# Optimization experiments

Measured on AMD Instinct MI355X. Metric: run time of the kernel, lower is better.

Reference implementation:

```python
import jax, jax.numpy as jnp
import numpy as np

N_NODES = 100000


def _gcn_layer(h_in, W, b, src, dst, norm, num_nodes):
    # PyG GCNConv: linear transform first, then normalized scatter-add aggregation
    h = h_in @ W                                   # [N, out_dim]
    msg = h[src] * norm[:, None]                   # gather + scale over edges
    out = jax.ops.segment_sum(msg, dst, num_segments=num_nodes)
    return out + b


def setup_inputs() -> dict:
    key = jax.random.key(0)
    k1, k2, k3, k4, k5 = jax.random.split(key, 5)
    d_in, d_hid, d_out = 128, 128, 128
    x = jax.random.normal(k1, (N_NODES, d_in), dtype=jnp.float32)
    edge_index = jax.random.randint(k2, (2, 1600000), 0, N_NODES, dtype=jnp.int64)
    # Glorot-ish init for weights, zeros for bias (as in GCNConv defaults)
    W1 = jax.random.normal(k3, (d_in, d_hid), dtype=jnp.float32) / np.sqrt(d_in)
    b1 = jnp.zeros((d_hid,), dtype=jnp.float32)
    W2 = jax.random.normal(k4, (d_hid, d_out), dtype=jnp.float32) / np.sqrt(d_hid)
    b2 = jnp.zeros((d_out,), dtype=jnp.float32)
    return {"x": x, "edge_index": edge_index, "W1": W1, "b1": b1, "W2": W2, "b2": b2}


def reference(x, edge_index, W1, b1, W2, b2):
    num_nodes = x.shape[0]
    # Add self-loops (GCNConv default add_self_loops=True)
    loop = jnp.arange(num_nodes, dtype=edge_index.dtype)
    src = jnp.concatenate([edge_index[0], loop])
    dst = jnp.concatenate([edge_index[1], loop])
    # Symmetric normalization: deg^{-1/2}[src] * deg^{-1/2}[dst]
    deg = jax.ops.segment_sum(jnp.ones_like(dst, dtype=x.dtype), dst, num_segments=num_nodes)
    dinv = jnp.where(deg > 0, jax.lax.rsqrt(deg), 0.0)
    norm = dinv[src] * dinv[dst]                   # [E + N]

    h = _gcn_layer(x, W1, b1, src, dst, norm, num_nodes)
    h = jax.nn.relu(h)                             # dropout is identity in eval mode
    out = _gcn_layer(h, W2, b2, src, dst, norm, num_nodes)
    return out
```

## Files before the change

### kernel.cpp

```cpp
#include <hip/hip_runtime.h>


#define DIM 128
#define CAP 192
typedef unsigned short ushort_t;
typedef unsigned int uint_t;
typedef __attribute__((ext_vector_type(8))) short bf16x8;
typedef __attribute__((ext_vector_type(4))) float f32x4;
typedef __attribute__((ext_vector_type(2))) float f32x2;

static __device__ __forceinline__ uint_t f2bf(float f) {
    union { float f; uint_t u; } c; c.f = f;
    uint_t u = c.u;
    return (u + 0x7FFFu + ((u >> 16) & 1u)) >> 16;
}
static __device__ __forceinline__ float bf2f(uint_t h) {
    union { uint_t u; float f; } c; c.u = h << 16;
    return c.f;
}
static __device__ __forceinline__ float as_f(uint_t u) {
    union { uint_t u; float f; } c; c.u = u;
    return c.f;
}
static __device__ __forceinline__ void gld16(const void* g, void* l) {
    __builtin_amdgcn_global_load_lds(
        (const __attribute__((address_space(1))) uint_t*)g,
        (__attribute__((address_space(3))) uint_t*)l, 16, 0, 0);
}

__global__ __launch_bounds__(256) void k_bin(const int* __restrict__ src,
                                             const int* __restrict__ dst,
                                             int* __restrict__ bcur,
                                             uint_t* __restrict__ stage,
                                             int E, int RB) {
    int e = blockIdx.x * 256 + threadIdx.x;
    if (e >= E) return;
    int slice = blockIdx.x & 31;
    int s = src[e], d = dst[e];
    int idx = slice * RB + (d >> 7);
    int c = atomicAdd(&bcur[idx], 1);
    if (c < CAP)
        stage[(size_t)idx * CAP + c] = (uint_t)((s << 7) | (d & 127));
}

__global__ __launch_bounds__(1024) void k_bscan(const int* __restrict__ bcur,
                                                int* __restrict__ bbase, int RB) {
    __shared__ int sdat[1024];
    int t = threadIdx.x;
    int v = 0;
    if (t < RB)
        #pragma unroll
        for (int s = 0; s < 32; ++s) v += min(bcur[s * RB + t], CAP);
    sdat[t] = v;
    __syncthreads();
    #pragma unroll
    for (int o = 1; o < 1024; o <<= 1) {
        int x = (t >= o) ? sdat[t - o] : 0;
        __syncthreads();
        sdat[t] += x;
        __syncthreads();
    }
    if (t < RB) bbase[t] = sdat[t] - v;
}

__global__ __launch_bounds__(256) void k_build(const uint_t* __restrict__ stage,
                                               const int* __restrict__ bcur,
                                               const int* __restrict__ bbase,
                                               int* __restrict__ off,
                                               float* __restrict__ dinv,
                                               int* __restrict__ csr_src,
                                               int RB, int N, int E) {
    __shared__ int scnt[33];
    __shared__ int cnt[128], excl[128], lcur[128];
    __shared__ uint_t ent[32 * CAP];
    int b = blockIdx.x, t = threadIdx.x;
    if (t < 32) scnt[t + 1] = min(bcur[t * RB + b], CAP);
    if (t == 0) scnt[0] = 0;
    if (t < 128) { cnt[t] = 0; lcur[t] = 0; }
    __syncthreads();
    if (t == 0)
        for (int s = 1; s <= 32; ++s) scnt[s] += scnt[s - 1];
    __syncthreads();
    int total = scnt[32];
    for (int s = 0; s < 32; ++s) {
        int c0 = scnt[s], c1 = scnt[s + 1];
        const uint_t* sp = stage + (size_t)(s * RB + b) * CAP - c0;
        for (int i = c0 + t; i < c1; i += 256) ent[i] = sp[i];
    }
    __syncthreads();
    for (int i = t; i < total; i += 256) atomicAdd(&cnt[ent[i] & 127], 1);
    __syncthreads();
    if (t < 128) excl[t] = cnt[t];
    __syncthreads();
    #pragma unroll
    for (int o = 1; o < 128; o <<= 1) {
        int x = 0;
        if (t < 128 && t >= o) x = excl[t - o];
        __syncthreads();
        if (t < 128) excl[t] += x;
        __syncthreads();
    }
    int base = bbase[b];
    if (t < 128) {
        excl[t] -= cnt[t];
        int node = (b << 7) + t;
        if (node < N) {
            off[node] = base + excl[t];
            dinv[node] = rsqrtf((float)cnt[t] + 1.0f);
        }
    }
    if (b == RB - 1 && t == 0) off[N] = E;
    __syncthreads();
    for (int i = t; i < total; i += 256) {
        uint_t v = ent[i];
        int dl = v & 127;
        int pos = base + excl[dl] + atomicAdd(&lcur[dl], 1);
        csr_src[pos] = (int)(v >> 7);
    }
}

__global__ __launch_bounds__(256) void k_prep(const float* __restrict__ W1,
                                              const float* __restrict__ W2,
                                              const float* __restrict__ x,
                                              short* __restrict__ whi,
                                              short* __restrict__ wlo,
                                              short* __restrict__ xhi,
                                              short* __restrict__ xlo,
                                              int N, int nxc) {
    int t = threadIdx.x;
    if (blockIdx.x < 16) {
        int g = blockIdx.x * 256 + t;
        int layer = g >> 11, c = g & 2047;
        const float* W = layer ? W2 : W1;
        int ks = c >> 9, nt = (c >> 6) & 7, l = c & 63;
        int q = l >> 4, m = l & 15;
        int n = nt * 16 + m;
        bf16x8 h8, l8;
        #pragma unroll
        for (int j = 0; j < 8; ++j) {
            int k = ks * 32 + q * 8 + j;
            float f = W[k * 128 + n];
            uint_t hb = f2bf(f);
            h8[j] = (short)hb;
            l8[j] = (short)f2bf(f - bf2f(hb));
        }
        ((bf16x8*)whi)[g] = h8;
        ((bf16x8*)wlo)[g] = l8;
    } else {
        int c = (blockIdx.x - 16) * 256 + t;
        if (c >= nxc) return;
        int rb = c >> 11, row = (c >> 4) & 127, cc = c & 15;
        int node = rb * 128 + row;
        bf16x8 h8 = {}, l8 = {};
        if (node < N) {
            f32x4 fa = __builtin_nontemporal_load((const f32x4*)x + node * 32 + cc * 2);
            f32x4 fb = __builtin_nontemporal_load((const f32x4*)x + node * 32 + cc * 2 + 1);
            float f[8] = {fa[0], fa[1], fa[2], fa[3], fb[0], fb[1], fb[2], fb[3]};
            #pragma unroll
            for (int j = 0; j < 8; ++j) {
                uint_t hb = f2bf(f[j]);
                h8[j] = (short)hb;
                l8[j] = (short)f2bf(f[j] - bf2f(hb));
            }
        }
        int pos = (cc & 8) | ((cc & 7) ^ (row & 7));
        int slot = rb * 2048 + row * 16 + pos;
        __builtin_nontemporal_store(h8, (bf16x8*)xhi + slot);
        __builtin_nontemporal_store(l8, (bf16x8*)xlo + slot);
    }
}

__global__ __launch_bounds__(256) void k_gemm(const short* __restrict__ afhi,
                                              const short* __restrict__ aflo,
                                              const short* __restrict__ wfhi,
                                              const short* __restrict__ wflo,
                                              const float* __restrict__ dinv,
                                              ushort_t* __restrict__ hout, int M) {
    __shared__ short AH[8192], AL[8192], WH[8192], WL[8192];
    const int t = threadIdx.x;
    const int rb = blockIdx.x;
    const int wv = t >> 6, l = t & 63;
    const int mb = (wv & 1) * 4;
    const int nbc = (wv >> 1) * 4;

    f32x4 acc[4][4];
    #pragma unroll
    for (int i = 0; i < 4; ++i)
        #pragma unroll
        for (int j = 0; j < 4; ++j)
            acc[i][j] = (f32x4){0.f, 0.f, 0.f, 0.f};

    #pragma unroll
    for (int kc = 0; kc < 2; ++kc) {
        if (kc) __syncthreads();
        {
            const short* ga = afhi + (size_t)rb * 16384;
            const short* gb = aflo + (size_t)rb * 16384;
            const short* gh = wfhi + 2 * kc * 4096;
            const short* gl = wflo + 2 * kc * 4096;
            #pragma unroll
            for (int i = 0; i < 4; ++i) {
                int idx = i * 256 + t;
                int goff = ((idx >> 3) * 16 + kc * 8 + (idx & 7)) * 8;
                gld16(ga + goff, AH + idx * 8);
                gld16(gb + goff, AL + idx * 8);
                gld16(gh + idx * 8, WH + idx * 8);
                gld16(gl + idx * 8, WL + idx * 8);
            }
        }
        __syncthreads();
        #pragma unroll
        for (int ksl = 0; ksl < 2; ++ksl) {
            bf16x8 ah[4], al[4];
            #pragma unroll
            for (int i = 0; i < 4; ++i) {
                int rowl = (mb + i) * 16 + (l & 15);
                int cA = ksl * 4 + (l >> 4);
                int sa = rowl * 64 + ((cA ^ (rowl & 7)) << 3);
                ah[i] = *(const bf16x8*)&AH[sa];
                al[i] = *(const bf16x8*)&AL[sa];
            }
            #pragma unroll
            for (int j = 0; j < 4; ++j) {
                bf16x8 bh = *(const bf16x8*)&WH[((ksl * 8 + nbc + j) * 64 + l) * 8];
                bf16x8 bl = *(const bf16x8*)&WL[((ksl * 8 + nbc + j) * 64 + l) * 8];
                #pragma unroll
                for (int i = 0; i < 4; ++i) {
                    acc[i][j] = __builtin_amdgcn_mfma_f32_16x16x32_bf16(ah[i], bh, acc[i][j], 0, 0, 0);
                    acc[i][j] = __builtin_amdgcn_mfma_f32_16x16x32_bf16(al[i], bh, acc[i][j], 0, 0, 0);
                    acc[i][j] = __builtin_amdgcn_mfma_f32_16x16x32_bf16(ah[i], bl, acc[i][j], 0, 0, 0);
                }
            }
        }
    }

    const int q = l >> 4, mm = l & 15;
    #pragma unroll
    for (int i = 0; i < 4; ++i)
        #pragma unroll
        for (int r = 0; r < 4; ++r) {
            int gr = rb * 128 + (wv & 1) * 64 + i * 16 + q * 4 + r;
            if (gr < M) {
                float di = dinv[gr];
                #pragma unroll
                for (int j = 0; j < 4; ++j)
                    hout[gr * 128 + nbc * 16 + j * 16 + mm] =
                        (ushort_t)f2bf(di * acc[i][j][r]);
            }
        }
}

template <int FRAG>
__global__ __launch_bounds__(256) void k_agg(const uint_t* __restrict__ h32,
                                             const int* __restrict__ off,
                                             const int* __restrict__ csr_src,
                                             const float* __restrict__ dinv,
                                             const float* __restrict__ bias,
                                             float* __restrict__ out,
                                             uint_t* __restrict__ fhi,
                                             uint_t* __restrict__ flo, int N) {
    int n = (blockIdx.x * 256 + threadIdx.x) >> 6;
    if (n >= N) return;
    int l = threadIdx.x & 63;
    const uint_t* hl = h32 + l;

    float di = dinv[n];
    f32x2 bv = *((const f32x2*)bias + l);
    uint_t sv = hl[(size_t)n << 6];
    float accx = as_f(sv << 16);
    float accy = as_f(sv & 0xffff0000u);

    int e = off[n], end = off[n + 1];
    for (; e + 16 <= end; e += 16) {
        int s[16]; uint_t v[16];
        #pragma unroll
        for (int u = 0; u < 16; ++u) s[u] = __builtin_nontemporal_load(&csr_src[e + u]);
        #pragma unroll
        for (int u = 0; u < 16; ++u) v[u] = hl[(size_t)s[u] << 6];
        #pragma unroll
        for (int u = 0; u < 16; ++u) {
            accx += as_f(v[u] << 16);
            accy += as_f(v[u] & 0xffff0000u);
        }
    }
    if (e + 8 <= end) {
        int s[8]; uint_t v[8];
        #pragma unroll
        for (int u = 0; u < 8; ++u) s[u] = __builtin_nontemporal_load(&csr_src[e + u]);
        #pragma unroll
        for (int u = 0; u < 8; ++u) v[u] = hl[(size_t)s[u] << 6];
        #pragma unroll
        for (int u = 0; u < 8; ++u) {
            accx += as_f(v[u] << 16);
            accy += as_f(v[u] & 0xffff0000u);
        }
        e += 8;
    }
    for (; e < end; ++e) {
        uint_t v = hl[(size_t)csr_src[e] << 6];
        accx += as_f(v << 16);
        accy += as_f(v & 0xffff0000u);
    }

    accx = di * accx + bv.x;
    accy = di * accy + bv.y;

    if (FRAG) {
        accx = fmaxf(accx, 0.f);
        accy = fmaxf(accy, 0.f);
        uint_t hx = f2bf(accx), hy = f2bf(accy);
        uint_t lx = f2bf(accx - bf2f(hx)), ly = f2bf(accy - bf2f(hy));
        int rb = n >> 7, row = n & 127, cc = l >> 2;
        int pos = (cc & 8) | ((cc & 7) ^ (row & 7));
        size_t iu = ((size_t)rb << 13) + row * 64 + pos * 4 + (l & 3);
        __builtin_nontemporal_store((hy << 16) | hx, &fhi[iu]);
        __builtin_nontemporal_store((ly << 16) | lx, &flo[iu]);
    } else {
        f32x2 o; o.x = accx; o.y = accy;
        __builtin_nontemporal_store(o, (f32x2*)out + ((size_t)n << 6) + l);
    }
}

extern "C" void kernel_launch(void* const* d_in, const int* in_sizes, int n_in,
                              void* d_out, int out_size, void* d_ws, size_t ws_size,
                              hipStream_t stream) {
    const float* x  = (const float*)d_in[0];
    const int*   ei = (const int*)d_in[1];
    const float* W1 = (const float*)d_in[2];
    const float* b1 = (const float*)d_in[3];
    const float* W2 = (const float*)d_in[4];
    const float* b2 = (const float*)d_in[5];
    float* out = (float*)d_out;

    const int N = in_sizes[0] / DIM;
    const int E = in_sizes[1] / 2;
    const int* src = ei;
    const int* dst = ei + E;
    const int RB = (N + 127) / 128;
    const int nxc = RB * 2048;

    char* w = (char*)d_ws;
    float* dinv    = (float*)(w);
    int*   bcur    = (int*)  (w + (1 << 19));
    int*   bbase   = (int*)  (w + (1 << 19) + (1 << 17));
    int*   off     = (int*)  (w + (3 << 19));
    short* whi     = (short*)(w + (1 << 21) + (1 << 13));
    short* wlo     = whi + 2 * 16384;
    int*   csr_src = (int*)  (w + ((size_t)5 << 19));
    short* fhi     = (short*)(w + ((size_t)17 << 20));
    short* flo     = (short*)(w + ((size_t)43 << 20));
    ushort_t* hbuf = (ushort_t*)(w + ((size_t)69 << 20));
    uint_t* stage  = (uint_t*)hbuf;

    const int B = 256;
    const int agg_grid = (N * 64 + B - 1) / B;

    hipMemsetAsync(bcur, 0, (size_t)32 * RB * 4, stream);
    k_prep<<<16 + (nxc + B - 1) / B, B, 0, stream>>>(W1, W2, x, whi, wlo,
                                                     fhi, flo, N, nxc);
    k_bin<<<(E + B - 1) / B, B, 0, stream>>>(src, dst, bcur, stage, E, RB);
    k_bscan<<<1, 1024, 0, stream>>>(bcur, bbase, RB);
    k_build<<<RB, B, 0, stream>>>(stage, bcur, bbase, off, dinv, csr_src,
                                  RB, N, E);
    k_gemm<<<RB, B, 0, stream>>>(fhi, flo, whi, wlo, dinv, hbuf, N);
    k_agg<1><<<agg_grid, B, 0, stream>>>((const uint_t*)hbuf, off, csr_src,
                                         dinv, b1, nullptr,
                                         (uint_t*)fhi, (uint_t*)flo, N);
    k_gemm<<<RB, B, 0, stream>>>(fhi, flo, whi + 16384, wlo + 16384, dinv, hbuf, N);
    k_agg<0><<<agg_grid, B, 0, stream>>>((const uint_t*)hbuf, off, csr_src,
                                         dinv, b2, out,
                                         nullptr, nullptr, N);
}
```

Baseline: 408.4 us.

## Split aggregation wave into two edge halves with 8-byte gathers; reorder A tiles by k-chunk

The aggregation kernel now has each 64-lane wave handle two edges per step. Each half-wave gathers a full 256-byte bf16 row using 8-byte loads per lane, and the two halves are combined with a cross-half shuffle at the end. The goal is fewer load instructions and more independent gathers in flight per wave. The fragment layout written by the conversion and aggregation kernels is also reorganised so each GEMM k-chunk is contiguous, letting the GEMM tile loads use plain linear offsets. In exchange, half the lanes sit idle in the epilogue and the shuffle reduction adds some work.

```diff
diff --git a/kernel.cpp b/kernel.cpp
--- a/kernel.cpp
+++ b/kernel.cpp
@@ -8,6 +8,7 @@
 typedef __attribute__((ext_vector_type(8))) short bf16x8;
 typedef __attribute__((ext_vector_type(4))) float f32x4;
 typedef __attribute__((ext_vector_type(2))) float f32x2;
+typedef __attribute__((ext_vector_type(2))) unsigned int u32x2;
 
 static __device__ __forceinline__ uint_t f2bf(float f) {
     union { float f; uint_t u; } c; c.f = f;
@@ -163,8 +164,7 @@
                 l8[j] = (short)f2bf(f[j] - bf2f(hb));
             }
         }
-        int pos = (cc & 8) | ((cc & 7) ^ (row & 7));
-        int slot = rb * 2048 + row * 16 + pos;
+        int slot = rb * 2048 + (cc >> 3) * 1024 + row * 8 + ((cc & 7) ^ (row & 7));
         __builtin_nontemporal_store(h8, (bf16x8*)xhi + slot);
         __builtin_nontemporal_store(l8, (bf16x8*)xlo + slot);
     }
@@ -194,18 +194,17 @@
     for (int kc = 0; kc < 2; ++kc) {
         if (kc) __syncthreads();
         {
-            const short* ga = afhi + (size_t)rb * 16384;
-            const short* gb = aflo + (size_t)rb * 16384;
-            const short* gh = wfhi + 2 * kc * 4096;
-            const short* gl = wflo + 2 * kc * 4096;
+            const short* ga = afhi + (size_t)rb * 16384 + kc * 8192;
+            const short* gb = aflo + (size_t)rb * 16384 + kc * 8192;
+            const short* gh = wfhi + kc * 8192;
+            const short* gl = wflo + kc * 8192;
             #pragma unroll
             for (int i = 0; i < 4; ++i) {
-                int idx = i * 256 + t;
-                int goff = ((idx >> 3) * 16 + kc * 8 + (idx & 7)) * 8;
-                gld16(ga + goff, AH + idx * 8);
-                gld16(gb + goff, AL + idx * 8);
-                gld16(gh + idx * 8, WH + idx * 8);
-                gld16(gl + idx * 8, WL + idx * 8);
+                int idx = (i * 256 + t) * 8;
+                gld16(ga + idx, AH + idx);
+                gld16(gb + idx, AL + idx);
+                gld16(gh + idx, WH + idx);
+                gld16(gl + idx, WL + idx);
             }
         }
         __syncthreads();
@@ -262,62 +261,73 @@
     int n = (blockIdx.x * 256 + threadIdx.x) >> 6;
     if (n >= N) return;
     int l = threadIdx.x & 63;
-    const uint_t* hl = h32 + l;
+    int half = l >> 5, c = l & 31;
+    const u32x2* hrow = (const u32x2*)h32 + c;
+
+    float ax = 0.f, ay = 0.f, az = 0.f, aw = 0.f;
+    if (!half) {
+        u32x2 sv = hrow[(size_t)n * 32];
+        ax = as_f(sv.x << 16); ay = as_f(sv.x & 0xffff0000u);
+        az = as_f(sv.y << 16); aw = as_f(sv.y & 0xffff0000u);
+    }
+
+    int e = off[n], end = off[n + 1];
+    for (; e + 32 <= end; e += 32) {
+        int s[16]; u32x2 v[16];
+        #pragma unroll
+        for (int u = 0; u < 16; ++u)
+            s[u] = __builtin_nontemporal_load(&csr_src[e + 2 * u + half]);
+        #pragma unroll
+        for (int u = 0; u < 16; ++u) v[u] = hrow[(size_t)s[u] * 32];
+        #pragma unroll
+        for (int u = 0; u < 16; ++u) {
+            ax += as_f(v[u].x << 16); ay += as_f(v[u].x & 0xffff0000u);
+            az += as_f(v[u].y << 16); aw += as_f(v[u].y & 0xffff0000u);
+        }
+    }
+    for (; e + 2 <= end; e += 2) {
+        int s = __builtin_nontemporal_load(&csr_src[e + half]);
+        u32x2 v = hrow[(size_t)s * 32];
+        ax += as_f(v.x << 16); ay += as_f(v.x & 0xffff0000u);
+        az += as_f(v.y << 16); aw += as_f(v.y & 0xffff0000u);
+    }
+    if (e < end && !half) {
+        int s = csr_src[e];
+        u32x2 v = hrow[(size_t)s * 32];
+        ax += as_f(v.x << 16); ay += as_f(v.x & 0xffff0000u);
+        az += as_f(v.y << 16); aw += as_f(v.y & 0xffff0000u);
+    }
+
+    ax += __shfl_xor(ax, 32, 64);
+    ay += __shfl_xor(ay, 32, 64);
+    az += __shfl_xor(az, 32, 64);
+    aw += __shfl_xor(aw, 32, 64);
+    if (half) return;
 
     float di = dinv[n];
-    f32x2 bv = *((const f32x2*)bias + l);
-    uint_t sv = hl[(size_t)n << 6];
-    float accx = as_f(sv << 16);
-    float accy = as_f(sv & 0xffff0000u);
-
-    int e = off[n], end = off[n + 1];
-    for (; e + 16 <= end; e += 16) {
-        int s[16]; uint_t v[16];
-        #pragma unroll
-        for (int u = 0; u < 16; ++u) s[u] = __builtin_nontemporal_load(&csr_src[e + u]);
-        #pragma unroll
-        for (int u = 0; u < 16; ++u) v[u] = hl[(size_t)s[u] << 6];
-        #pragma unroll
-        for (int u = 0; u < 16; ++u) {
-            accx += as_f(v[u] << 16);
-            accy += as_f(v[u] & 0xffff0000u);
-        }
-    }
-    if (e + 8 <= end) {
-        int s[8]; uint_t v[8];
-        #pragma unroll
-        for (int u = 0; u < 8; ++u) s[u] = __builtin_nontemporal_load(&csr_src[e + u]);
-        #pragma unroll
-        for (int u = 0; u < 8; ++u) v[u] = hl[(size_t)s[u] << 6];
-        #pragma unroll
-        for (int u = 0; u < 8; ++u) {
-            accx += as_f(v[u] << 16);
-            accy += as_f(v[u] & 0xffff0000u);
-        }
-        e += 8;
-    }
-    for (; e < end; ++e) {
-        uint_t v = hl[(size_t)csr_src[e] << 6];
-        accx += as_f(v << 16);
-        accy += as_f(v & 0xffff0000u);
-    }
-
-    accx = di * accx + bv.x;
-    accy = di * accy + bv.y;
+    f32x4 bv = *((const f32x4*)bias + c);
+    ax = di * ax + bv[0];
+    ay = di * ay + bv[1];
+    az = di * az + bv[2];
+    aw = di * aw + bv[3];
 
     if (FRAG) {
-        accx = fmaxf(accx, 0.f);
-        accy = fmaxf(accy, 0.f);
-        uint_t hx = f2bf(accx), hy = f2bf(accy);
-        uint_t lx = f2bf(accx - bf2f(hx)), ly = f2bf(accy - bf2f(hy));
-        int rb = n >> 7, row = n & 127, cc = l >> 2;
-        int pos = (cc & 8) | ((cc & 7) ^ (row & 7));
-        size_t iu = ((size_t)rb << 13) + row * 64 + pos * 4 + (l & 3);
-        __builtin_nontemporal_store((hy << 16) | hx, &fhi[iu]);
-        __builtin_nontemporal_store((ly << 16) | lx, &flo[iu]);
+        ax = fmaxf(ax, 0.f); ay = fmaxf(ay, 0.f);
+        az = fmaxf(az, 0.f); aw = fmaxf(aw, 0.f);
+        uint_t w0h = (f2bf(ay) << 16) | f2bf(ax);
+        uint_t w1h = (f2bf(aw) << 16) | f2bf(az);
+        uint_t w0l = (f2bf(ay - bf2f(f2bf(ay))) << 16) | f2bf(ax - bf2f(f2bf(ax)));
+        uint_t w1l = (f2bf(aw - bf2f(f2bf(aw))) << 16) | f2bf(az - bf2f(f2bf(az)));
+        int rb = n >> 7, row = n & 127;
+        int p7 = ((c >> 1) & 7) ^ (row & 7);
+        size_t i2 = (size_t)rb * 4096 + (c >> 4) * 2048 + row * 16 + p7 * 2 + (c & 1);
+        u32x2 vh; vh.x = w0h; vh.y = w1h;
+        u32x2 vl; vl.x = w0l; vl.y = w1l;
+        __builtin_nontemporal_store(vh, (u32x2*)fhi + i2);
+        __builtin_nontemporal_store(vl, (u32x2*)flo + i2);
     } else {
-        f32x2 o; o.x = accx; o.y = accy;
-        __builtin_nontemporal_store(o, (f32x2*)out + ((size_t)n << 6) + l);
+        f32x4 o; o[0] = ax; o[1] = ay; o[2] = az; o[3] = aw;
+        __builtin_nontemporal_store(o, (f32x4*)out + (size_t)n * 32 + c);
     }
 }
 
```

Measured after the change: 552.9 us. 1.35x slower.
